# Kernel optimization log

Measured on AMD Instinct MI355X. Metric: run time of the kernel, lower is better.

## Reference

```python
import jax, jax.numpy as jnp
import numpy as np

B, T, N_EMBED, HEADSIZE = 16, 2048, 1024, 128


def setup_inputs() -> dict:
    key = jax.random.key(0)
    kx, kq, kk, kv = jax.random.split(key, 4)
    x = jax.random.normal(kx, (B, T, N_EMBED), dtype=jnp.float32)
    # nn.Linear(n_embed, headsize, bias=False): y = x @ W, W stored [n_embed, headsize]
    s = (1.0 / np.sqrt(N_EMBED)).astype(np.float32)
    Wq = jax.random.normal(kq, (N_EMBED, HEADSIZE), dtype=jnp.float32) * s
    Wk = jax.random.normal(kk, (N_EMBED, HEADSIZE), dtype=jnp.float32) * s
    Wv = jax.random.normal(kv, (N_EMBED, HEADSIZE), dtype=jnp.float32) * s
    return {"x": x, "Wq": Wq, "Wk": Wk, "Wv": Wv}


def reference(x, Wq, Wk, Wv):
    Bsz, Tlen, C = x.shape
    q = x @ Wq  # [B, T, H]
    k = x @ Wk  # [B, T, H]
    v = x @ Wv  # [B, T, H]
    scale = C ** (-0.5)  # NOTE: original scales by n_embed**-0.5, not headsize**-0.5
    wt = jnp.einsum('bqh,bkh->bqk', q, k) * scale  # [B, T, T]
    causal = jnp.tril(jnp.ones((Tlen, Tlen), dtype=bool))
    wt = jnp.where(causal, wt, -jnp.inf)
    wt = jax.nn.softmax(wt, axis=-1)
    # dropout is identity in eval mode
    out = jnp.einsum('bqk,bkh->bqh', wt, v)  # [B, T, H]
    return out
```

## Files before the change

kernel.cpp:

```cpp
#include <hip/hip_runtime.h>
#include <hip/hip_bf16.h>

#define BATCH 16
#define TLEN 2048
#define CDIM 1024
#define HDIM 128

typedef __attribute__((ext_vector_type(8))) short bf16x8;
typedef __attribute__((ext_vector_type(4))) float f32x4;
typedef __attribute__((ext_vector_type(16))) float f32x16;
typedef __attribute__((ext_vector_type(4))) unsigned short u16x4;
typedef __attribute__((ext_vector_type(8))) unsigned short u16x8;

static __device__ __forceinline__ unsigned short f2bf(float f) {
    __hip_bfloat16 h = __float2bfloat16(f);
    return *(unsigned short*)&h;
}
static __device__ __forceinline__ unsigned pkbf(float a, float b) {
    return (unsigned)f2bf(a) | ((unsigned)f2bf(b) << 16);
}
static __device__ __forceinline__ int part_offs(int qc) {
    return qc + ((qc * qc - 2 * qc + (qc & 1)) >> 2);
}

__global__ __launch_bounds__(256) void pack_w(
    const float* __restrict__ Wq, const float* __restrict__ Wk,
    const float* __restrict__ Wv, unsigned short* __restrict__ wtb)
{
    const int which = blockIdx.y;
    const float* W = (which == 0) ? Wq : (which == 1) ? Wk : Wv;
    const int n = blockIdx.x >> 2;
    const int k = (blockIdx.x & 3) * 256 + threadIdx.x;
    wtb[((size_t)which * 128 + n) * 1024 + k] = f2bf(W[(size_t)k * 128 + n]);
}

__global__ __launch_bounds__(256) void qkv_mfma(
    const float* __restrict__ x, const unsigned short* __restrict__ wtb,
    unsigned short* __restrict__ qb, unsigned short* __restrict__ kb,
    unsigned short* __restrict__ vtb)
{
    __shared__ unsigned short As[128 * 64];
    __shared__ unsigned short Bs[128 * 64];

    const int bid = blockIdx.x;
    const int xcd = bid & 7, s = bid >> 3;
    const int m0 = (xcd * 32 + s / 3) * 128;
    const int nt = s % 3;

    const int tid  = threadIdx.x;
    const int lane = tid & 63, wid = tid >> 6;
    const int wm = wid >> 1, wn = wid & 1;
    const int c = lane & 15, g = lane >> 4;
    const unsigned short* Wp = wtb + (size_t)nt * 128 * 1024;

    f32x4 acc[4][4];
#pragma unroll
    for (int i = 0; i < 4; ++i)
#pragma unroll
        for (int j = 0; j < 4; ++j) acc[i][j] = (f32x4){0.f, 0.f, 0.f, 0.f};

    bf16x8 av[4], bv[4];

#pragma unroll
    for (int i = 0; i < 4; ++i) {
        const int j = tid + i * 256, row = j >> 3, ch = j & 7;
        const float* src = x + (size_t)(m0 + row) * CDIM + ch * 8;
        float4 f0 = *(const float4*)src, f1 = *(const float4*)(src + 4);
        bf16x8 t;
        t[0]=f2bf(f0.x); t[1]=f2bf(f0.y); t[2]=f2bf(f0.z); t[3]=f2bf(f0.w);
        t[4]=f2bf(f1.x); t[5]=f2bf(f1.y); t[6]=f2bf(f1.z); t[7]=f2bf(f1.w);
        av[i] = t;
        bv[i] = *(const bf16x8*)(Wp + (size_t)row * 1024 + ch * 8);
    }
#pragma unroll
    for (int i = 0; i < 4; ++i) {
        const int j = tid + i * 256, row = j >> 3, ch = j & 7;
        const int off = row * 128 + ((ch * 16) ^ ((row & 7) << 4));
        *(bf16x8*)((char*)As + off) = av[i];
        *(bf16x8*)((char*)Bs + off) = bv[i];
    }
    __syncthreads();

#pragma unroll 1
    for (int kt = 0; kt < 16; ++kt) {
        if (kt < 15) {
            const int k0 = (kt + 1) * 64;
#pragma unroll
            for (int i = 0; i < 4; ++i) {
                const int j = tid + i * 256, row = j >> 3, ch = j & 7;
                const float* src = x + (size_t)(m0 + row) * CDIM + k0 + ch * 8;
                float4 f0 = *(const float4*)src, f1 = *(const float4*)(src + 4);
                bf16x8 t;
                t[0]=f2bf(f0.x); t[1]=f2bf(f0.y); t[2]=f2bf(f0.z); t[3]=f2bf(f0.w);
                t[4]=f2bf(f1.x); t[5]=f2bf(f1.y); t[6]=f2bf(f1.z); t[7]=f2bf(f1.w);
                av[i] = t;
                bv[i] = *(const bf16x8*)(Wp + (size_t)row * 1024 + k0 + ch * 8);
            }
        }

#pragma unroll
        for (int ks = 0; ks < 2; ++ks) {
            bf16x8 af[4], bf[4];
#pragma unroll
            for (int mf = 0; mf < 4; ++mf) {
                const int row = wm * 64 + mf * 16 + c;
                const int off = row * 128 + ((ks * 64 + g * 16) ^ ((row & 7) << 4));
                af[mf] = *(const bf16x8*)((char*)As + off);
            }
#pragma unroll
            for (int nf = 0; nf < 4; ++nf) {
                const int row = wn * 64 + nf * 16 + c;
                const int off = row * 128 + ((ks * 64 + g * 16) ^ ((row & 7) << 4));
                bf[nf] = *(const bf16x8*)((char*)Bs + off);
            }
#pragma unroll
            for (int mf = 0; mf < 4; ++mf)
#pragma unroll
                for (int nf = 0; nf < 4; ++nf)
                    acc[mf][nf] = __builtin_amdgcn_mfma_f32_16x16x32_bf16(
                        af[mf], bf[nf], acc[mf][nf], 0, 0, 0);
        }

        if (kt < 15) {
            __syncthreads();
#pragma unroll
            for (int i = 0; i < 4; ++i) {
                const int j = tid + i * 256, row = j >> 3, ch = j & 7;
                const int off = row * 128 + ((ch * 16) ^ ((row & 7) << 4));
                *(bf16x8*)((char*)As + off) = av[i];
                *(bf16x8*)((char*)Bs + off) = bv[i];
            }
            __syncthreads();
        }
    }

    const int mb = m0 + wm * 64, nb = wn * 64;
    if (nt == 0) {
#pragma unroll
        for (int mf = 0; mf < 4; ++mf)
#pragma unroll
            for (int nf = 0; nf < 4; ++nf)
#pragma unroll
                for (int r = 0; r < 4; ++r) {
                    const int m = mb + mf * 16 + g * 4 + r;
                    const int n = nb + nf * 16 + c;
                    qb[(size_t)m * HDIM + n] = f2bf(acc[mf][nf][r] * 0.03125f);
                }
    } else if (nt == 1) {
#pragma unroll
        for (int mf = 0; mf < 4; ++mf)
#pragma unroll
            for (int nf = 0; nf < 4; ++nf)
#pragma unroll
                for (int r = 0; r < 4; ++r) {
                    const int m = mb + mf * 16 + g * 4 + r;
                    const int n = nb + nf * 16 + c;
                    kb[(size_t)m * HDIM + n] = f2bf(acc[mf][nf][r]);
                }
    } else {
#pragma unroll
        for (int mf = 0; mf < 4; ++mf)
#pragma unroll
            for (int nf = 0; nf < 4; ++nf) {
                const int m = mb + mf * 16 + g * 4;
                const int b = m >> 11, t = m & (TLEN - 1);
                const int n = nb + nf * 16 + c;
                u16x4 o;
                o[0] = f2bf(acc[mf][nf][0]); o[1] = f2bf(acc[mf][nf][1]);
                o[2] = f2bf(acc[mf][nf][2]); o[3] = f2bf(acc[mf][nf][3]);
                *(u16x4*)(vtb + ((size_t)b * HDIM + n) * TLEN + t) = o;
            }
    }
}

__global__ __launch_bounds__(256, 2) void attn_partial(
    const short* __restrict__ qb, const short* __restrict__ kb,
    const short* __restrict__ vtb,
    unsigned short* __restrict__ Opart, float* __restrict__ mpart,
    float* __restrict__ lpart)
{
    const int kc = blockIdx.x;
    const int qc = blockIdx.y;
    const int b  = blockIdx.z;
    if (kc > (qc >> 1)) return;
    const int kv_base = kc * 256;
    const int qrel = qc * 128 - kv_base;
    int NT = ((qrel + 127) >> 6) + 1; if (NT > 4) NT = 4;

    __shared__ unsigned short Ks[2][64 * 128];
    __shared__ unsigned short Vs[2][128 * 64];

    const int tid  = threadIdx.x;
    const int wid  = tid >> 6;
    const int lane = tid & 63;
    const int c5 = lane & 31, hi = lane >> 5;
    const int q0w = qc * 128 + wid * 32;
    const int qg  = q0w + c5;
    const int pidx = b * 72 + part_offs(qc) + kc;

    const short* Kb  = kb  + (size_t)b * TLEN * HDIM;
    const short* Vtb = vtb + (size_t)b * HDIM * TLEN;

    bf16x8 qf[8];
#pragma unroll
    for (int ks = 0; ks < 8; ++ks)
        qf[ks] = *(const bf16x8*)(qb + ((size_t)b * TLEN + qg) * HDIM + ks * 16 + hi * 8);

    bf16x8 kst[4], vst[4];

#define GLOAD(kv0_)                                                          \
    {                                                                        \
        _Pragma("unroll")                                                    \
        for (int it = 0; it < 4; ++it) {                                     \
            const int o = tid * 16 + it * 4096;                              \
            const int kr = o >> 8, kcb = o & 0xF0;                           \
            kst[it] = *(const bf16x8*)((const char*)Kb +                     \
                        (size_t)((kv0_) + kr) * 256 + kcb);                  \
            const int vr = o >> 7, vcb = o & 0x70;                           \
            vst[it] = *(const bf16x8*)((const char*)Vtb +                    \
                        (size_t)vr * (TLEN * 2) + (size_t)(kv0_) * 2 + vcb); \
        }                                                                    \
    }
#define SSTORE(bi_)                                                          \
    {                                                                        \
        _Pragma("unroll")                                                    \
        for (int it = 0; it < 4; ++it) {                                     \
            const int o = tid * 16 + it * 4096;                              \
            const int kr = o >> 8, kcb = o & 0xF0;                           \
            *(bf16x8*)((char*)Ks[bi_] + kr * 256 + (kcb ^ ((kr & 7) << 4))) = kst[it]; \
            const int vr = o >> 7, vcb = o & 0x70;                           \
            *(bf16x8*)((char*)Vs[bi_] + vr * 128 + (vcb ^ ((vr & 7) << 4))) = vst[it]; \
        }                                                                    \
    }

    GLOAD(kv_base);
    SSTORE(0);
    __syncthreads();

    f32x16 oacc[4];
#pragma unroll
    for (int i = 0; i < 4; ++i)
#pragma unroll
        for (int r = 0; r < 16; ++r) oacc[i][r] = 0.f;
    float m_r = -1e30f;
    float l_r = 0.f;

#pragma unroll 1
    for (int t = 0; t < NT; ++t) {
        const int bi = t & 1;
        if (t + 1 < NT) GLOAD(kv_base + 64 * (t + 1));

        const int kv0 = kv_base + 64 * t;
        if (kv0 <= q0w + 31) {
            f32x16 s0, s1;
#pragma unroll
            for (int r = 0; r < 16; ++r) { s0[r] = 0.f; s1[r] = 0.f; }
#pragma unroll
            for (int ks = 0; ks < 8; ++ks) {
                const int col = ks * 32 + hi * 16;
                const int off0 = c5 * 256 + (col ^ ((c5 & 7) << 4));
                const int off1 = (32 + c5) * 256 + (col ^ ((c5 & 7) << 4));
                bf16x8 a0 = *(const bf16x8*)((char*)Ks[bi] + off0);
                bf16x8 a1 = *(const bf16x8*)((char*)Ks[bi] + off1);
                s0 = __builtin_amdgcn_mfma_f32_32x32x16_bf16(a0, qf[ks], s0, 0, 0, 0);
                s1 = __builtin_amdgcn_mfma_f32_32x32x16_bf16(a1, qf[ks], s1, 0, 0, 0);
            }

            if (kv0 + 63 > q0w) {
#pragma unroll
                for (int r = 0; r < 16; ++r) {
                    const int key0 = kv0 + (r & 3) + 8 * (r >> 2) + 4 * hi;
                    if (key0 > qg)      s0[r] = -INFINITY;
                    if (key0 + 32 > qg) s1[r] = -INFINITY;
                }
            }

            float t8[8];
#pragma unroll
            for (int i = 0; i < 8; ++i)
                t8[i] = fmaxf(fmaxf(s0[2*i], s0[2*i+1]), fmaxf(s1[2*i], s1[2*i+1]));
            float smax = fmaxf(fmaxf(fmaxf(t8[0], t8[1]), fmaxf(t8[2], t8[3])),
                               fmaxf(fmaxf(t8[4], t8[5]), fmaxf(t8[6], t8[7])));
            smax = fmaxf(smax, __shfl_xor(smax, 32));

            const bool defer = __all(smax - m_r <= 8.0f);
            const float mnew = defer ? m_r : fmaxf(m_r, smax);
            if (!defer) {
                const float alpha = __expf(m_r - mnew);
                l_r *= alpha;
#pragma unroll
                for (int hb = 0; hb < 4; ++hb) oacc[hb] = oacc[hb] * alpha;
            }
            m_r = mnew;

#pragma unroll
            for (int r = 0; r < 16; ++r) {
                s0[r] = __expf(s0[r] - mnew);
                s1[r] = __expf(s1[r] - mnew);
            }
            float a8[8];
#pragma unroll
            for (int i = 0; i < 8; ++i)
                a8[i] = (s0[2*i] + s0[2*i+1]) + (s1[2*i] + s1[2*i+1]);
            float psum = ((a8[0] + a8[1]) + (a8[2] + a8[3])) +
                         ((a8[4] + a8[5]) + (a8[6] + a8[7]));
            psum += __shfl_xor(psum, 32);
            l_r += psum;

            bf16x8 pa[4];
#pragma unroll
            for (int kb2 = 0; kb2 < 2; ++kb2) {
#pragma unroll
                for (int par = 0; par < 2; ++par) {
                    const int e = par * 8;
                    float v0, v1, v2, v3, v4, v5, v6, v7;
                    if (kb2 == 0) {
                        v0=s0[e+0]; v1=s0[e+1]; v2=s0[e+2]; v3=s0[e+3];
                        v4=s0[e+4]; v5=s0[e+5]; v6=s0[e+6]; v7=s0[e+7];
                    } else {
                        v0=s1[e+0]; v1=s1[e+1]; v2=s1[e+2]; v3=s1[e+3];
                        v4=s1[e+4]; v5=s1[e+5]; v6=s1[e+6]; v7=s1[e+7];
                    }
                    const unsigned w0 = pkbf(v0, v1), w1 = pkbf(v2, v3);
                    const unsigned w2 = pkbf(v4, v5), w3 = pkbf(v6, v7);
                    const unsigned X0 = hi ? w0 : w2;
                    const unsigned X1 = hi ? w1 : w3;
                    const unsigned R0 = (unsigned)__shfl_xor((int)X0, 32);
                    const unsigned R1 = (unsigned)__shfl_xor((int)X1, 32);
                    union { unsigned w[4]; bf16x8 v; } uu;
                    uu.w[0] = hi ? R0 : w0;  uu.w[1] = hi ? R1 : w1;
                    uu.w[2] = hi ? w2 : R0;  uu.w[3] = hi ? w3 : R1;
                    pa[kb2 * 2 + par] = uu.v;
                }
            }

#pragma unroll
            for (int hb = 0; hb < 4; ++hb) {
                const int row = hb * 32 + c5;
#pragma unroll
                for (int ks = 0; ks < 4; ++ks) {
                    const int off = row * 128 + ((ks * 32 + hi * 16) ^ ((row & 7) << 4));
                    bf16x8 va = *(const bf16x8*)((char*)Vs[bi] + off);
                    oacc[hb] = __builtin_amdgcn_mfma_f32_32x32x16_bf16(va, pa[ks], oacc[hb], 0, 0, 0);
                }
            }
        }

        if (t + 1 < NT) {
            SSTORE(bi ^ 1);
            __syncthreads();
        }
    }

    __syncthreads();
    char* sl = (char*)Ks + wid * 8192;
#pragma unroll
    for (int hb = 0; hb < 4; ++hb)
#pragma unroll
        for (int rq = 0; rq < 4; ++rq) {
            u16x4 o4;
            o4[0] = f2bf(oacc[hb][rq * 4 + 0]);
            o4[1] = f2bf(oacc[hb][rq * 4 + 1]);
            o4[2] = f2bf(oacc[hb][rq * 4 + 2]);
            o4[3] = f2bf(oacc[hb][rq * 4 + 3]);
            const int off = c5 * 256 + ((hb * 64 + rq * 16 + hi * 8) ^ ((c5 & 7) << 4));
            *(u16x4*)(sl + off) = o4;
        }
    asm volatile("s_waitcnt lgkmcnt(0)" ::: "memory");
    __builtin_amdgcn_sched_barrier(0);

    const int qr = lane >> 1, hf = lane & 1;
    unsigned short* Og = Opart + (size_t)pidx * 128 * 128 +
                         (size_t)(wid * 32 + qr) * 128 + hf * 64;
#pragma unroll
    for (int i = 0; i < 8; ++i) {
        const int off = qr * 256 + ((hf * 128 + i * 16) ^ ((qr & 7) << 4));
        *(u16x8*)(Og + i * 8) = *(const u16x8*)(sl + off);
    }
    if (hi == 0) {
        mpart[(size_t)pidx * 128 + wid * 32 + c5] = m_r;
        lpart[(size_t)pidx * 128 + wid * 32 + c5] = l_r;
    }
#undef GLOAD
#undef SSTORE
}

__global__ __launch_bounds__(256) void attn_combine(
    const unsigned short* __restrict__ Opart, const float* __restrict__ mpart,
    const float* __restrict__ lpart, float* __restrict__ out)
{
    const int qc = blockIdx.x;
    const int b  = blockIdx.y;
    const int n  = (qc >> 1) + 1;
    const int base = b * 72 + part_offs(qc);
    const int t   = threadIdx.x;
    const int row = t >> 1;
    const int d0  = (t & 1) * 64;

    float M = -INFINITY;
    for (int p = 0; p < n; ++p)
        M = fmaxf(M, mpart[(size_t)(base + p) * 128 + row]);
    float L = 0.f;
    for (int p = 0; p < n; ++p)
        L += __expf(mpart[(size_t)(base + p) * 128 + row] - M) *
             lpart[(size_t)(base + p) * 128 + row];

    float acc[64];
#pragma unroll
    for (int i = 0; i < 64; ++i) acc[i] = 0.f;

    for (int p = 0; p < n; ++p) {
        const float w = __expf(mpart[(size_t)(base + p) * 128 + row] - M);
        const bf16x8* src = (const bf16x8*)(Opart +
            ((size_t)(base + p) * 128 + row) * 128 + d0);
#pragma unroll
        for (int j = 0; j < 8; ++j) {
            bf16x8 v = src[j];
#pragma unroll
            for (int e = 0; e < 8; ++e) {
                union { unsigned u; float f; } x;
                x.u = ((unsigned)(unsigned short)v[e]) << 16;
                acc[j * 8 + e] += w * x.f;
            }
        }
    }

    const float invL = 1.f / L;
    float4* dst = (float4*)(out + ((size_t)(b * TLEN + qc * 128 + row)) * 128 + d0);
#pragma unroll
    for (int i = 0; i < 16; ++i)
        dst[i] = make_float4(acc[4*i] * invL, acc[4*i+1] * invL,
                             acc[4*i+2] * invL, acc[4*i+3] * invL);
}

extern "C" void kernel_launch(void* const* d_in, const int* in_sizes, int n_in,
                              void* d_out, int out_size, void* d_ws, size_t ws_size,
                              hipStream_t stream)
{
    const float* x  = (const float*)d_in[0];
    const float* Wq = (const float*)d_in[1];
    const float* Wk = (const float*)d_in[2];
    const float* Wv = (const float*)d_in[3];
    float* outp = (float*)d_out;

    const size_t per = (size_t)BATCH * TLEN * HDIM;
    unsigned short* qb  = (unsigned short*)d_ws;
    unsigned short* kb  = qb + per;
    unsigned short* vtb = kb + per;
    unsigned short* wtb = vtb + per;
    unsigned short* Opart = wtb + 384 * 1024;
    float* mpart = (float*)(Opart + (size_t)1152 * 128 * 128);
    float* lpart = mpart + (size_t)1152 * 128;

    dim3 gw(512, 3);
    pack_w<<<gw, 256, 0, stream>>>(Wq, Wk, Wv, wtb);

    qkv_mfma<<<768, 256, 0, stream>>>(x, wtb, qb, kb, vtb);

    dim3 g2(8, 16, BATCH);
    attn_partial<<<g2, 256, 0, stream>>>((const short*)qb, (const short*)kb,
                                         (const short*)vtb, Opart, mpart, lpart);

    dim3 g3(16, BATCH);
    attn_combine<<<g3, 256, 0, stream>>>(Opart, mpart, lpart, outp);
}
```

Baseline: 138.4 us.

## Pre-convert x to bf16 and stage QKV GEMM tiles via direct global-to-LDS loads

Adds a separate kernel that converts x to bf16 into a workspace buffer, which aliases the Opart region. The QKV GEMM then loads its tiles with global_load_lds straight into shared memory instead of staging through registers. This drops the register round trip and the XOR swizzle, and the GEMM now reads half the bytes of x. The cost is an extra full pass over x (read fp32, write bf16), possible LDS bank conflicts from the unswizzled layout, and loss of the prefetch-compute overlap, since the next tile is issued only after compute finishes. It also wraps the attention MFMA blocks in s_setprio hints.

```diff
diff --git a/kernel.cpp b/kernel.cpp
--- a/kernel.cpp
+++ b/kernel.cpp
@@ -23,6 +23,27 @@
     return qc + ((qc * qc - 2 * qc + (qc & 1)) >> 2);
 }
 
+typedef const __attribute__((address_space(1))) unsigned int* gas_t;
+typedef __attribute__((address_space(3))) unsigned int* las_t;
+static __device__ __forceinline__ void gl_lds16(const void* g, void* l) {
+    __builtin_amdgcn_global_load_lds((gas_t)g, (las_t)l, 16, 0, 0);
+}
+
+__global__ __launch_bounds__(256) void x2bf(
+    const float* __restrict__ x, unsigned short* __restrict__ xb)
+{
+    const size_t n8 = (size_t)BATCH * TLEN * CDIM / 8;
+    const size_t stride = (size_t)gridDim.x * 256;
+    for (size_t i = (size_t)blockIdx.x * 256 + threadIdx.x; i < n8; i += stride) {
+        const float4 f0 = ((const float4*)x)[2 * i];
+        const float4 f1 = ((const float4*)x)[2 * i + 1];
+        u16x8 o;
+        o[0] = f2bf(f0.x); o[1] = f2bf(f0.y); o[2] = f2bf(f0.z); o[3] = f2bf(f0.w);
+        o[4] = f2bf(f1.x); o[5] = f2bf(f1.y); o[6] = f2bf(f1.z); o[7] = f2bf(f1.w);
+        *(u16x8*)(xb + i * 8) = o;
+    }
+}
+
 __global__ __launch_bounds__(256) void pack_w(
     const float* __restrict__ Wq, const float* __restrict__ Wk,
     const float* __restrict__ Wv, unsigned short* __restrict__ wtb)
@@ -35,7 +56,7 @@
 }
 
 __global__ __launch_bounds__(256) void qkv_mfma(
-    const float* __restrict__ x, const unsigned short* __restrict__ wtb,
+    const unsigned short* __restrict__ xb, const unsigned short* __restrict__ wtb,
     unsigned short* __restrict__ qb, unsigned short* __restrict__ kb,
     unsigned short* __restrict__ vtb)
 {
@@ -53,50 +74,34 @@
     const int c = lane & 15, g = lane >> 4;
     const unsigned short* Wp = wtb + (size_t)nt * 128 * 1024;
 
+    const int lrow = lane >> 3;
+    const int lcol = (lane & 7) * 8;
+
     f32x4 acc[4][4];
 #pragma unroll
     for (int i = 0; i < 4; ++i)
 #pragma unroll
         for (int j = 0; j < 4; ++j) acc[i][j] = (f32x4){0.f, 0.f, 0.f, 0.f};
 
-    bf16x8 av[4], bv[4];
-
-#pragma unroll
-    for (int i = 0; i < 4; ++i) {
-        const int j = tid + i * 256, row = j >> 3, ch = j & 7;
-        const float* src = x + (size_t)(m0 + row) * CDIM + ch * 8;
-        float4 f0 = *(const float4*)src, f1 = *(const float4*)(src + 4);
-        bf16x8 t;
-        t[0]=f2bf(f0.x); t[1]=f2bf(f0.y); t[2]=f2bf(f0.z); t[3]=f2bf(f0.w);
-        t[4]=f2bf(f1.x); t[5]=f2bf(f1.y); t[6]=f2bf(f1.z); t[7]=f2bf(f1.w);
-        av[i] = t;
-        bv[i] = *(const bf16x8*)(Wp + (size_t)row * 1024 + ch * 8);
-    }
-#pragma unroll
-    for (int i = 0; i < 4; ++i) {
-        const int j = tid + i * 256, row = j >> 3, ch = j & 7;
-        const int off = row * 128 + ((ch * 16) ^ ((row & 7) << 4));
-        *(bf16x8*)((char*)As + off) = av[i];
-        *(bf16x8*)((char*)Bs + off) = bv[i];
-    }
-    __syncthreads();
+#define STAGE(k0_)                                                            \
+    {                                                                         \
+        _Pragma("unroll")                                                     \
+        for (int i = 0; i < 4; ++i) {                                         \
+            const int seg = wid * 4 + i;                                      \
+            const unsigned short* ga = xb +                                   \
+                (size_t)(m0 + seg * 8 + lrow) * CDIM + (k0_) + lcol;          \
+            const unsigned short* gb = Wp +                                   \
+                (size_t)(seg * 8 + lrow) * CDIM + (k0_) + lcol;               \
+            gl_lds16(ga, (char*)As + seg * 1024);                             \
+            gl_lds16(gb, (char*)Bs + seg * 1024);                             \
+        }                                                                     \
+    }
+
+    STAGE(0);
 
 #pragma unroll 1
     for (int kt = 0; kt < 16; ++kt) {
-        if (kt < 15) {
-            const int k0 = (kt + 1) * 64;
-#pragma unroll
-            for (int i = 0; i < 4; ++i) {
-                const int j = tid + i * 256, row = j >> 3, ch = j & 7;
-                const float* src = x + (size_t)(m0 + row) * CDIM + k0 + ch * 8;
-                float4 f0 = *(const float4*)src, f1 = *(const float4*)(src + 4);
-                bf16x8 t;
-                t[0]=f2bf(f0.x); t[1]=f2bf(f0.y); t[2]=f2bf(f0.z); t[3]=f2bf(f0.w);
-                t[4]=f2bf(f1.x); t[5]=f2bf(f1.y); t[6]=f2bf(f1.z); t[7]=f2bf(f1.w);
-                av[i] = t;
-                bv[i] = *(const bf16x8*)(Wp + (size_t)row * 1024 + k0 + ch * 8);
-            }
-        }
+        __syncthreads();
 
 #pragma unroll
         for (int ks = 0; ks < 2; ++ks) {
@@ -104,14 +109,12 @@
 #pragma unroll
             for (int mf = 0; mf < 4; ++mf) {
                 const int row = wm * 64 + mf * 16 + c;
-                const int off = row * 128 + ((ks * 64 + g * 16) ^ ((row & 7) << 4));
-                af[mf] = *(const bf16x8*)((char*)As + off);
+                af[mf] = *(const bf16x8*)((char*)As + row * 128 + ks * 64 + g * 16);
             }
 #pragma unroll
             for (int nf = 0; nf < 4; ++nf) {
                 const int row = wn * 64 + nf * 16 + c;
-                const int off = row * 128 + ((ks * 64 + g * 16) ^ ((row & 7) << 4));
-                bf[nf] = *(const bf16x8*)((char*)Bs + off);
+                bf[nf] = *(const bf16x8*)((char*)Bs + row * 128 + ks * 64 + g * 16);
             }
 #pragma unroll
             for (int mf = 0; mf < 4; ++mf)
@@ -123,14 +126,7 @@
 
         if (kt < 15) {
             __syncthreads();
-#pragma unroll
-            for (int i = 0; i < 4; ++i) {
-                const int j = tid + i * 256, row = j >> 3, ch = j & 7;
-                const int off = row * 128 + ((ch * 16) ^ ((row & 7) << 4));
-                *(bf16x8*)((char*)As + off) = av[i];
-                *(bf16x8*)((char*)Bs + off) = bv[i];
-            }
-            __syncthreads();
+            STAGE((kt + 1) * 64);
         }
     }
 
@@ -171,6 +167,7 @@
                 *(u16x4*)(vtb + ((size_t)b * HDIM + n) * TLEN + t) = o;
             }
     }
+#undef STAGE
 }
 
 __global__ __launch_bounds__(256, 2) void attn_partial(
@@ -255,6 +252,7 @@
             f32x16 s0, s1;
 #pragma unroll
             for (int r = 0; r < 16; ++r) { s0[r] = 0.f; s1[r] = 0.f; }
+            __builtin_amdgcn_s_setprio(1);
 #pragma unroll
             for (int ks = 0; ks < 8; ++ks) {
                 const int col = ks * 32 + hi * 16;
@@ -265,6 +263,7 @@
                 s0 = __builtin_amdgcn_mfma_f32_32x32x16_bf16(a0, qf[ks], s0, 0, 0, 0);
                 s1 = __builtin_amdgcn_mfma_f32_32x32x16_bf16(a1, qf[ks], s1, 0, 0, 0);
             }
+            __builtin_amdgcn_s_setprio(0);
 
             if (kv0 + 63 > q0w) {
 #pragma unroll
@@ -334,6 +333,7 @@
                 }
             }
 
+            __builtin_amdgcn_s_setprio(1);
 #pragma unroll
             for (int hb = 0; hb < 4; ++hb) {
                 const int row = hb * 32 + c5;
@@ -344,6 +344,7 @@
                     oacc[hb] = __builtin_amdgcn_mfma_f32_32x32x16_bf16(va, pa[ks], oacc[hb], 0, 0, 0);
                 }
             }
+            __builtin_amdgcn_s_setprio(0);
         }
 
         if (t + 1 < NT) {
@@ -448,14 +449,17 @@
     unsigned short* kb  = qb + per;
     unsigned short* vtb = kb + per;
     unsigned short* wtb = vtb + per;
-    unsigned short* Opart = wtb + 384 * 1024;
+    unsigned short* xbuf = wtb + 384 * 1024;
+    unsigned short* Opart = xbuf;
     float* mpart = (float*)(Opart + (size_t)1152 * 128 * 128);
     float* lpart = mpart + (size_t)1152 * 128;
 
+    x2bf<<<2048, 256, 0, stream>>>(x, xbuf);
+
     dim3 gw(512, 3);
     pack_w<<<gw, 256, 0, stream>>>(Wq, Wk, Wv, wtb);
 
-    qkv_mfma<<<768, 256, 0, stream>>>(x, wtb, qb, kb, vtb);
+    qkv_mfma<<<768, 256, 0, stream>>>(xbuf, wtb, qb, kb, vtb);
 
     dim3 g2(8, 16, BATCH);
     attn_partial<<<g2, 256, 0, stream>>>((const short*)qb, (const short*)kb,
```

Measured after the change: 164.6 us. +18.9%, slower.
